# Performance work log

Measured on AMD Instinct MI355X. Metric: run time of the kernel, lower is better.

Reference implementation:

```python
import jax, jax.numpy as jnp
import numpy as np

B, N, C_IN, C_OUT, K = 8, 2048, 64, 128, 20
EPS = 1e-5  # BatchNorm2d default eps


def setup_inputs() -> dict:
    key = jax.random.key(0)
    k1, k2 = jax.random.split(key, 2)
    x = jax.random.normal(k1, (B, C_IN, N), dtype=jnp.float32)
    fan_in = 2 * C_IN
    W = jax.random.normal(k2, (C_OUT, 2 * C_IN), dtype=jnp.float32) / np.sqrt(fan_in).astype(np.float32)
    b = jnp.zeros((C_OUT,), jnp.float32)
    gamma = jnp.ones((C_OUT,), jnp.float32)
    beta = jnp.zeros((C_OUT,), jnp.float32)
    return {"x": x, "W": W, "b": b, "gamma": gamma, "beta": beta}


def reference(x, W, b, gamma, beta):
    # x: (B, C_in, N) -> points (B, N, C_in)
    pts = jnp.transpose(x, (0, 2, 1))
    # pairwise squared L2 distances (B, N, N)
    sq = jnp.sum(pts * pts, axis=-1)
    dist = sq[:, :, None] + sq[:, None, :] - 2.0 * jnp.einsum('bnc,bmc->bnm', pts, pts)
    # knn: top-k of negated distance -> k nearest neighbors (includes self)
    _, nn_idx = jax.lax.top_k(-dist, K)  # (B, N, K)
    # gather neighbor features per batch: (B, N, K, C_in)
    neigh = jax.vmap(lambda p, i: p[i])(pts, nn_idx)
    central = pts[:, :, None, :]  # (B, N, 1, C_in)
    edge = jnp.concatenate(
        [jnp.broadcast_to(central, neigh.shape), neigh - central], axis=-1
    )  # (B, N, K, 2*C_in)
    # 1x1 conv == channelwise linear: (B, N, K, C_out)
    y = jnp.einsum('bnkc,oc->bnko', edge, W) + b
    # BatchNorm2d (training mode): stats over batch + spatial dims, biased var
    mean = jnp.mean(y, axis=(0, 1, 2))
    var = jnp.var(y, axis=(0, 1, 2))
    y = (y - mean) * jax.lax.rsqrt(var + EPS) * gamma + beta
    y = jax.nn.relu(y)
    y = jnp.max(y, axis=2)  # max over k neighbors -> (B, N, C_out)
    return jnp.transpose(y, (0, 2, 1))[..., None]  # (B, C_out, N, 1)
```

## Files before the change

kernel.cpp:

```cpp
#include <hip/hip_runtime.h>
#include <cstdint>
#include <cstddef>

#define NPTS 2048
#define BATCH 8
#define CIN 64
#define CO 128
#define KNN 20
#define KSEL 24
#define NSPLIT 4
#define MKP 25

typedef short s16x8 __attribute__((ext_vector_type(8)));
typedef unsigned short u16x8 __attribute__((ext_vector_type(8)));
typedef float f32x4 __attribute__((ext_vector_type(4)));

__device__ inline unsigned short f2bf_rne(float x) {
  unsigned u = __float_as_uint(x);
  unsigned r = (u + 0x7FFFu + ((u >> 16) & 1u)) >> 16;
  return (unsigned short)r;
}
__device__ inline float bf2f(unsigned short h) {
  return __uint_as_float(((unsigned)h) << 16);
}
__device__ inline unsigned med3u(unsigned a, unsigned b, unsigned c) {
  unsigned d;
  asm("v_med3_u32 %0, %1, %2, %3" : "=v"(d) : "v"(a), "v"(b), "v"(c));
  return d;
}

__global__ __launch_bounds__(256) void prep_kernel(
    const float* __restrict__ x, float* __restrict__ P,
    unsigned short* __restrict__ PG, float* __restrict__ SQ,
    float* __restrict__ STATS) {
  __shared__ float tile[64 * 33];
  const int b = blockIdx.y, hb = blockIdx.x;
  const int n0 = hb * 32;
  const int tid = threadIdx.x;
  if (b == 0 && hb == 0) {
    for (int t = tid; t < 5 * CO; t += 256) STATS[t] = 0.f;
  }
  const float* xb = x + (size_t)b * CIN * NPTS;
#pragma unroll
  for (int j = 0; j < 8; ++j) {
    int e = j * 256 + tid;
    int c = e >> 5, nl = e & 31;
    tile[c * 33 + nl] = xb[(size_t)c * NPTS + n0 + nl];
  }
  __syncthreads();
  float* Pb = P + (size_t)b * NPTS * CIN;
#pragma unroll
  for (int j = 0; j < 8; ++j) {
    int e = j * 256 + tid;
    int nl = e >> 6, c = e & 63;
    Pb[(size_t)(n0 + nl) * CIN + c] = tile[c * 33 + nl];
  }
  if (tid < 32) {
    float acc = 0.f;
#pragma unroll
    for (int c = 0; c < 64; ++c) {
      float v = tile[c * 33 + tid];
      acc = fmaf(v, v, acc);
    }
    SQ[(size_t)b * NPTS + n0 + tid] = acc;
  }
  const size_t tbase = (size_t)(b * 32 + (n0 >> 6)) * 8192;
  {
    const int rl = tid >> 3, kc = tid & 7;
    const int grow = (n0 & 63) + rl;
    const int frag = ((grow >> 4) << 1) | (kc >> 2);
    const int lidx = (grow & 15) | ((kc & 3) << 4);
    s16x8 hi8, lo8;
#pragma unroll
    for (int e = 0; e < 8; ++e) {
      float v = tile[(kc * 8 + e) * 33 + rl];
      unsigned short hb_ = f2bf_rne(v);
      float hf = bf2f(hb_);
      unsigned short lb = f2bf_rne(v - hf);
      hi8[e] = (short)hb_;
      lo8[e] = (short)lb;
    }
    size_t co = (size_t)(frag * 64 + lidx) * 8;
    *(s16x8*)(PG + tbase + co) = hi8;
    *(s16x8*)(PG + tbase + 4096 + co) = lo8;
  }
}

__global__ __launch_bounds__(256, 4) void knn_part_kernel(
    const unsigned short* __restrict__ PG, const float* __restrict__ SQ,
    unsigned* __restrict__ POOLS) {
  const int b = blockIdx.z;
  const int cs = blockIdx.y;
  const int n0 = blockIdx.x * 64;
  const int tid = threadIdx.x;
  const int lane = tid & 63, w = tid >> 6;
  const int qi = w * 16 + (lane & 15);
  const int sub = lane >> 4;
  const int T0 = cs * 8;

  __shared__ unsigned mk[64 * 4 * MKP];

  const size_t tqb = (size_t)(b * 32 + (n0 >> 6)) * 8192;
  const s16x8 qhi0 = *(const s16x8*)(PG + tqb + (size_t)((w * 2 + 0) * 64 + lane) * 8);
  const s16x8 qhi1 = *(const s16x8*)(PG + tqb + (size_t)((w * 2 + 1) * 64 + lane) * 8);
  const s16x8 qlo0 = *(const s16x8*)(PG + tqb + 4096 + (size_t)((w * 2 + 0) * 64 + lane) * 8);
  const s16x8 qlo1 = *(const s16x8*)(PG + tqb + 4096 + (size_t)((w * 2 + 1) * 64 + lane) * 8);

  unsigned hk[KSEL];
#pragma unroll
  for (int s = 0; s < KSEL; ++s) hk[s] = 0xFFFFFFFFu;

#pragma unroll 1
  for (int t = 0; t < 8; ++t) {
    const int T = T0 + t;
    const unsigned short* tb = PG + (size_t)(b * 32 + T) * 8192;
#pragma unroll
    for (int rt = 0; rt < 4; ++rt) {
      const s16x8 ahi0 = *(const s16x8*)(tb + (size_t)((rt * 2 + 0) * 64 + lane) * 8);
      const s16x8 ahi1 = *(const s16x8*)(tb + (size_t)((rt * 2 + 1) * 64 + lane) * 8);
      const s16x8 alo0 = *(const s16x8*)(tb + 4096 + (size_t)((rt * 2 + 0) * 64 + lane) * 8);
      const s16x8 alo1 = *(const s16x8*)(tb + 4096 + (size_t)((rt * 2 + 1) * 64 + lane) * 8);
      f32x4 acc0 = {0.f, 0.f, 0.f, 0.f};
      f32x4 acc1 = {0.f, 0.f, 0.f, 0.f};
      acc0 = __builtin_amdgcn_mfma_f32_16x16x32_bf16(alo0, qhi0, acc0, 0, 0, 0);
      acc1 = __builtin_amdgcn_mfma_f32_16x16x32_bf16(alo1, qhi1, acc1, 0, 0, 0);
      acc0 = __builtin_amdgcn_mfma_f32_16x16x32_bf16(ahi0, qlo0, acc0, 0, 0, 0);
      acc1 = __builtin_amdgcn_mfma_f32_16x16x32_bf16(ahi1, qlo1, acc1, 0, 0, 0);
      acc0 = __builtin_amdgcn_mfma_f32_16x16x32_bf16(ahi0, qhi0, acc0, 0, 0, 0);
      acc1 = __builtin_amdgcn_mfma_f32_16x16x32_bf16(ahi1, qhi1, acc1, 0, 0, 0);
      const float4 sq4 = *(const float4*)(SQ + b * NPTS + T * 64 + rt * 16 + sub * 4);
      const float sqa[4] = {sq4.x, sq4.y, sq4.z, sq4.w};
      const int mbase = T * 64 + rt * 16 + sub * 4;
#pragma unroll
      for (int r = 0; r < 4; ++r) {
        float d = fmaf(acc0[r] + acc1[r], -2.0f, sqa[r]);
        unsigned u = __float_as_uint(d);
        unsigned ord = u ^ (unsigned)(((int)u >> 31) | 0x80000000);
        unsigned key = (ord & 0xFFFFF800u) | (unsigned)(mbase + r);
#pragma unroll
        for (int s = KSEL - 1; s >= 1; --s) hk[s] = med3u(hk[s - 1], hk[s], key);
        hk[0] = hk[0] < key ? hk[0] : key;
      }
    }
  }

#pragma unroll
  for (int s = 0; s < KSEL; ++s) mk[(qi * 4 + sub) * MKP + s] = hk[s];
  __syncthreads();

  if (sub == 0) {
    const unsigned* bl = mk + qi * 4 * MKP;
    unsigned* pq = POOLS + ((size_t)(b * NPTS + n0 + qi) * NSPLIT + cs) * KSEL;
    int p0 = 0, p1 = 0, p2 = 0, p3 = 0;
#pragma unroll 1
    for (int s = 0; s < KSEL; ++s) {
      unsigned k0 = (p0 < KSEL) ? bl[0 * MKP + p0] : 0xFFFFFFFFu;
      unsigned k1 = (p1 < KSEL) ? bl[1 * MKP + p1] : 0xFFFFFFFFu;
      unsigned k2 = (p2 < KSEL) ? bl[2 * MKP + p2] : 0xFFFFFFFFu;
      unsigned k3 = (p3 < KSEL) ? bl[3 * MKP + p3] : 0xFFFFFFFFu;
      unsigned bk = k0; int bs = 0;
      if (k1 < bk) { bk = k1; bs = 1; }
      if (k2 < bk) { bk = k2; bs = 2; }
      if (k3 < bk) { bk = k3; bs = 3; }
      pq[s] = bk;
      if (bs == 0) ++p0; else if (bs == 1) ++p1; else if (bs == 2) ++p2; else ++p3;
    }
  }
}

__global__ __launch_bounds__(256) void merge_proj_kernel(
    const float* __restrict__ P, const float* __restrict__ W,
    const unsigned* __restrict__ POOLS, int* __restrict__ IDX,
    float* __restrict__ U, unsigned short* __restrict__ Vh) {
  __shared__ __align__(16) char smem[35072];
  const int tid = threadIdx.x;

  if (blockIdx.x < 1024) {
    const int blk = blockIdx.x;
    const int r0 = (blk >> 2) * 64;
    const int o0 = (blk & 3) * 32;
    const int og = tid & 3;
    const int nl = tid >> 2;
    float* Pt = (float*)smem;
    float* Wu_s = Pt + 64 * 65;
    float* Wd_s = Wu_s + 64 * 36;

#pragma unroll
    for (int j = 0; j < 16; ++j) {
      int e = j * 256 + tid;
      int c = e & 63, rl = e >> 6;
      Pt[rl * 65 + c] = P[((size_t)(r0 + rl) << 6) + c];
    }
#pragma unroll
    for (int j = 0; j < 8; ++j) {
      int e = j * 256 + tid;
      int c = e & 63, ol = e >> 6;
      float w1 = W[(size_t)(o0 + ol) * 128 + c];
      float w2 = W[(size_t)(o0 + ol) * 128 + 64 + c];
      Wu_s[c * 36 + ol] = w1 - w2;
      Wd_s[c * 36 + ol] = w2;
    }
    __syncthreads();

    float au[8] = {0,0,0,0,0,0,0,0};
    float av[8] = {0,0,0,0,0,0,0,0};
#pragma unroll 4
    for (int c = 0; c < 64; ++c) {
      float p = Pt[nl * 65 + c];
      const float* wu = Wu_s + c * 36 + og * 8;
      const float* wd = Wd_s + c * 36 + og * 8;
      float4 u0 = *(const float4*)wu;
      float4 u1 = *(const float4*)(wu + 4);
      float4 dd0 = *(const float4*)wd;
      float4 dd1 = *(const float4*)(wd + 4);
      au[0] = fmaf(p, u0.x, au[0]); au[1] = fmaf(p, u0.y, au[1]);
      au[2] = fmaf(p, u0.z, au[2]); au[3] = fmaf(p, u0.w, au[3]);
      au[4] = fmaf(p, u1.x, au[4]); au[5] = fmaf(p, u1.y, au[5]);
      au[6] = fmaf(p, u1.z, au[6]); au[7] = fmaf(p, u1.w, au[7]);
      av[0] = fmaf(p, dd0.x, av[0]); av[1] = fmaf(p, dd0.y, av[1]);
      av[2] = fmaf(p, dd0.z, av[2]); av[3] = fmaf(p, dd0.w, av[3]);
      av[4] = fmaf(p, dd1.x, av[4]); av[5] = fmaf(p, dd1.y, av[5]);
      av[6] = fmaf(p, dd1.z, av[6]); av[7] = fmaf(p, dd1.w, av[7]);
    }
    size_t ob = (size_t)(r0 + nl) * CO + o0 + og * 8;
    float4 s0 = {au[0], au[1], au[2], au[3]};
    float4 s1 = {au[4], au[5], au[6], au[7]};
    *(float4*)(U + ob) = s0;
    *(float4*)(U + ob + 4) = s1;
    u16x8 hv;
#pragma unroll
    for (int j = 0; j < 8; ++j) hv[j] = f2bf_rne(av[j]);
    *(u16x8*)(Vh + ob) = hv;
  } else {
    const int mblk = blockIdx.x - 1024;
    const int qi = tid >> 3, st = tid & 7;
    const int r0 = mblk * 32;
    const int r = r0 + qi;
    const int b = r >> 11;

    unsigned* lists = (unsigned*)smem;
    unsigned* pool = lists + 32 * NSPLIT * KSEL;
    double* cd = (double*)(pool + 32 * KSEL);

    {
      const unsigned* src = POOLS + (size_t)r0 * NSPLIT * KSEL;
      for (int t = tid; t < 32 * NSPLIT * KSEL; t += 256) lists[t] = src[t];
    }
    __syncthreads();

    if (st == 0) {
      const unsigned* bl = lists + qi * NSPLIT * KSEL;
      unsigned* pq = pool + qi * KSEL;
      int p0 = 0, p1 = 0, p2 = 0, p3 = 0;
#pragma unroll 1
      for (int s = 0; s < KSEL; ++s) {
        unsigned k0 = (p0 < KSEL) ? bl[0 * KSEL + p0] : 0xFFFFFFFFu;
        unsigned k1 = (p1 < KSEL) ? bl[1 * KSEL + p1] : 0xFFFFFFFFu;
        unsigned k2 = (p2 < KSEL) ? bl[2 * KSEL + p2] : 0xFFFFFFFFu;
        unsigned k3 = (p3 < KSEL) ? bl[3 * KSEL + p3] : 0xFFFFFFFFu;
        unsigned bk = k0; int bs = 0;
        if (k1 < bk) { bk = k1; bs = 1; }
        if (k2 < bk) { bk = k2; bs = 2; }
        if (k3 < bk) { bk = k3; bs = 3; }
        pq[s] = bk;
        if (bs == 0) ++p0; else if (bs == 1) ++p1; else if (bs == 2) ++p2; else ++p3;
      }
    }
    __syncthreads();

    const float* qrow = P + ((size_t)r << 6);
    float4 q4[16];
#pragma unroll
    for (int t = 0; t < 16; ++t) q4[t] = ((const float4*)qrow)[t];
#pragma unroll 1
    for (int j = 0; j < 3; ++j) {
      int cand = st * 3 + j;
      unsigned key = pool[qi * KSEL + cand];
      int m = (int)(key & 0x7FFu);
      const float* prow = P + ((size_t)(b * NPTS + m) << 6);
      double a0 = 0.0, a1 = 0.0;
#pragma unroll
      for (int t = 0; t < 16; ++t) {
        float4 pv = ((const float4*)prow)[t];
        double d0 = (double)pv.x - (double)q4[t].x;
        double d1 = (double)pv.y - (double)q4[t].y;
        double d2 = (double)pv.z - (double)q4[t].z;
        double d3 = (double)pv.w - (double)q4[t].w;
        a0 = fma(d1, d1, fma(d0, d0, a0));
        a1 = fma(d3, d3, fma(d2, d2, a1));
      }
      cd[qi * KSEL + cand] = a0 + a1;
    }
    __syncthreads();

    int* op = IDX + (size_t)r * KNN;
#pragma unroll 1
    for (int j = 0; j < 3; ++j) {
      int cand = st * 3 + j;
      double dv = cd[qi * KSEL + cand];
      int iv = (int)(pool[qi * KSEL + cand] & 0x7FFu);
      int rk = 0;
#pragma unroll 1
      for (int t = 0; t < KSEL; ++t) {
        double dt = cd[qi * KSEL + t];
        int it = (int)(pool[qi * KSEL + t] & 0x7FFu);
        rk += ((dt < dv) || (dt == dv && it < iv)) ? 1 : 0;
      }
      if (rk < KNN) op[rk] = iv;
    }
  }
}

__global__ __launch_bounds__(256) void gstats_kernel(
    const float* __restrict__ U, const unsigned short* __restrict__ Vh,
    const int* __restrict__ IDX, unsigned short* __restrict__ Zh,
    float* __restrict__ STATS) {
  const int r0 = blockIdx.x * 16;
  const int tid = threadIdx.x;
  const int og = tid & 15, nl = tid >> 4;
  const int r = r0 + nl;
  const int b = r >> 11;
  const unsigned short* Vb = Vh + ((size_t)b << 11) * CO;

  __shared__ int ii[16 * KNN];
  __shared__ float red[4][5][128];

  for (int t = tid; t < 16 * KNN; t += 256) ii[t] = IDX[(size_t)r0 * KNN + t];
  __syncthreads();

  float vmax[8], svr[8], svvr[8];
#pragma unroll
  for (int j = 0; j < 8; ++j) { vmax[j] = -3.4e38f; svr[j] = 0.f; svvr[j] = 0.f; }
#pragma unroll 4
  for (int k = 0; k < KNN; ++k) {
    int idx = ii[nl * KNN + k];
    u16x8 hv = *(const u16x8*)(Vb + (size_t)idx * CO + og * 8);
#pragma unroll
    for (int j = 0; j < 8; ++j) {
      float v = bf2f((unsigned short)hv[j]);
      vmax[j] = fmaxf(vmax[j], v);
      svr[j] += v;
      svvr[j] = fmaf(v, v, svvr[j]);
    }
  }
  size_t ob = (size_t)r * CO + og * 8;
  float4 u0 = *(const float4*)(U + ob);
  float4 u1 = *(const float4*)(U + ob + 4);
  float uu[8] = {u0.x, u0.y, u0.z, u0.w, u1.x, u1.y, u1.z, u1.w};
  u16x8 zh;
#pragma unroll
  for (int j = 0; j < 8; ++j) zh[j] = f2bf_rne(uu[j] + vmax[j]);
  *(u16x8*)(Zh + ob) = zh;

  float pu[8], puu[8], psv[8], pusv[8], psvv[8];
#pragma unroll
  for (int j = 0; j < 8; ++j) {
    pu[j] = uu[j];
    puu[j] = uu[j] * uu[j];
    psv[j] = svr[j];
    pusv[j] = uu[j] * svr[j];
    psvv[j] = svvr[j];
  }
#pragma unroll
  for (int j = 0; j < 8; ++j) {
    pu[j]   += __shfl_xor(pu[j], 16);   pu[j]   += __shfl_xor(pu[j], 32);
    puu[j]  += __shfl_xor(puu[j], 16);  puu[j]  += __shfl_xor(puu[j], 32);
    psv[j]  += __shfl_xor(psv[j], 16);  psv[j]  += __shfl_xor(psv[j], 32);
    pusv[j] += __shfl_xor(pusv[j], 16); pusv[j] += __shfl_xor(pusv[j], 32);
    psvv[j] += __shfl_xor(psvv[j], 16); psvv[j] += __shfl_xor(psvv[j], 32);
  }
  const int w = tid >> 6;
  if ((tid & 0x30) == 0) {
#pragma unroll
    for (int j = 0; j < 8; ++j) {
      int c = og * 8 + j;
      red[w][0][c] = pu[j];  red[w][1][c] = puu[j];  red[w][2][c] = psv[j];
      red[w][3][c] = pusv[j]; red[w][4][c] = psvv[j];
    }
  }
  __syncthreads();
  if (tid < 128) {
#pragma unroll
    for (int s = 0; s < 5; ++s) {
      float v4 = red[0][s][tid] + red[1][s][tid] + red[2][s][tid] + red[3][s][tid];
      atomicAdd(&STATS[s * CO + tid], v4);
    }
  }
}

__global__ __launch_bounds__(256) void out_kernel(
    const unsigned short* __restrict__ Zh, const float* __restrict__ STATS,
    const float* __restrict__ bias, const float* __restrict__ gamma,
    const float* __restrict__ beta, float* __restrict__ out) {
  const int n0 = blockIdx.x * 64, o0 = blockIdx.y * 32, b = blockIdx.z;
  const int tid = threadIdx.x;
  __shared__ float tile[64 * 33];
  __shared__ float fs[32], ft[32];
  if (tid < 32) {
    const int o = o0 + tid;
    const float M = (float)(BATCH * NPTS * KNN);
    const float Kf = (float)KNN;
    float su = STATS[0 * CO + o], suu = STATS[1 * CO + o], ssv = STATS[2 * CO + o];
    float susv = STATS[3 * CO + o], ssvv = STATS[4 * CO + o];
    float bo = bias[o];
    float lin = (Kf * su + ssv) / M;
    float mean = lin + bo;
    float ey2 = (Kf * suu + ssvv + 2.0f * susv) / M + 2.0f * bo * lin + bo * bo;
    float var = ey2 - mean * mean;
    float scale = gamma[o] * rsqrtf(var + 1e-5f);
    fs[tid] = scale;
    ft[tid] = (bo - mean) * scale + beta[o];
  }
#pragma unroll
  for (int j = 0; j < 8; ++j) {
    int e = j * 256 + tid;
    int ol = e & 31, nl = e >> 5;
    tile[nl * 33 + ol] = bf2f(Zh[(size_t)(b * NPTS + n0 + nl) * CO + o0 + ol]);
  }
  __syncthreads();
#pragma unroll
  for (int j = 0; j < 8; ++j) {
    int e = j * 256 + tid;
    int nl = e & 63, ol = e >> 6;
    float v = fmaf(tile[nl * 33 + ol], fs[ol], ft[ol]);
    out[(size_t)(b * CO + o0 + ol) * NPTS + n0 + nl] = fmaxf(v, 0.0f);
  }
}

extern "C" void kernel_launch(void* const* d_in, const int* in_sizes, int n_in,
                              void* d_out, int out_size, void* d_ws, size_t ws_size,
                              hipStream_t stream) {
  const float* x = (const float*)d_in[0];
  const float* W = (const float*)d_in[1];
  const float* bias = (const float*)d_in[2];
  const float* gamma = (const float*)d_in[3];
  const float* beta = (const float*)d_in[4];
  float* out = (float*)d_out;
  float* ws = (float*)d_ws;

  const size_t NR = (size_t)BATCH * NPTS;
  size_t off = 0;
  float* P = ws + off;                      off += NR * CIN;
  unsigned short* PG = (unsigned short*)(ws + off); off += NR * CIN;
  float* SQ = ws + off;                     off += NR;
  int* IDX = (int*)(ws + off);              off += NR * KNN;
  float* U = ws + off;                      off += NR * CO;
  unsigned short* Vh = (unsigned short*)(ws + off); off += NR * CO / 2;
  unsigned* POOLS = (unsigned*)(ws + off);  off += NR * NSPLIT * KSEL;
  float* STATS = ws + off;                  off += 5 * CO;
  unsigned short* Zh = (unsigned short*)ws;
  if (ws_size < off * sizeof(float)) return;

  prep_kernel<<<dim3(NPTS / 32, BATCH), 256, 0, stream>>>(x, P, PG, SQ, STATS);
  knn_part_kernel<<<dim3(NPTS / 64, NSPLIT, BATCH), 256, 0, stream>>>(PG, SQ, POOLS);
  merge_proj_kernel<<<dim3(1024 + NR / 32), 256, 0, stream>>>(P, W, POOLS, IDX, U, Vh);
  gstats_kernel<<<dim3(NR / 16), 256, 0, stream>>>(U, Vh, IDX, Zh, STATS);
  out_kernel<<<dim3(NPTS / 64, CO / 32, BATCH), 256, 0, stream>>>(Zh, STATS, bias, gamma, beta, out);
}
```

Measured before the change: 135.7 us.

## Store U projection in bf16 and chain kNN MFMAs into one accumulator

The U projection buffer is now written and read as bf16 instead of fp32, which halves its global memory traffic between merge_proj and gstats. In the kNN kernel the two independent MFMA accumulators become a single serial chain, which removes one add per element and some registers. The kNN kernel also drops its minimum-occupancy launch bound. Rounding U to bf16 loses precision in the BN statistics and outputs, and the serial MFMA chain creates a longer dependency between instructions.

```diff
diff --git a/kernel.cpp b/kernel.cpp
--- a/kernel.cpp
+++ b/kernel.cpp
@@ -86,7 +86,7 @@
   }
 }
 
-__global__ __launch_bounds__(256, 4) void knn_part_kernel(
+__global__ __launch_bounds__(256) void knn_part_kernel(
     const unsigned short* __restrict__ PG, const float* __restrict__ SQ,
     unsigned* __restrict__ POOLS) {
   const int b = blockIdx.z;
@@ -120,20 +120,19 @@
       const s16x8 ahi1 = *(const s16x8*)(tb + (size_t)((rt * 2 + 1) * 64 + lane) * 8);
       const s16x8 alo0 = *(const s16x8*)(tb + 4096 + (size_t)((rt * 2 + 0) * 64 + lane) * 8);
       const s16x8 alo1 = *(const s16x8*)(tb + 4096 + (size_t)((rt * 2 + 1) * 64 + lane) * 8);
-      f32x4 acc0 = {0.f, 0.f, 0.f, 0.f};
-      f32x4 acc1 = {0.f, 0.f, 0.f, 0.f};
-      acc0 = __builtin_amdgcn_mfma_f32_16x16x32_bf16(alo0, qhi0, acc0, 0, 0, 0);
-      acc1 = __builtin_amdgcn_mfma_f32_16x16x32_bf16(alo1, qhi1, acc1, 0, 0, 0);
-      acc0 = __builtin_amdgcn_mfma_f32_16x16x32_bf16(ahi0, qlo0, acc0, 0, 0, 0);
-      acc1 = __builtin_amdgcn_mfma_f32_16x16x32_bf16(ahi1, qlo1, acc1, 0, 0, 0);
-      acc0 = __builtin_amdgcn_mfma_f32_16x16x32_bf16(ahi0, qhi0, acc0, 0, 0, 0);
-      acc1 = __builtin_amdgcn_mfma_f32_16x16x32_bf16(ahi1, qhi1, acc1, 0, 0, 0);
+      f32x4 acc = {0.f, 0.f, 0.f, 0.f};
+      acc = __builtin_amdgcn_mfma_f32_16x16x32_bf16(alo0, qhi0, acc, 0, 0, 0);
+      acc = __builtin_amdgcn_mfma_f32_16x16x32_bf16(ahi0, qlo0, acc, 0, 0, 0);
+      acc = __builtin_amdgcn_mfma_f32_16x16x32_bf16(ahi0, qhi0, acc, 0, 0, 0);
+      acc = __builtin_amdgcn_mfma_f32_16x16x32_bf16(alo1, qhi1, acc, 0, 0, 0);
+      acc = __builtin_amdgcn_mfma_f32_16x16x32_bf16(ahi1, qlo1, acc, 0, 0, 0);
+      acc = __builtin_amdgcn_mfma_f32_16x16x32_bf16(ahi1, qhi1, acc, 0, 0, 0);
       const float4 sq4 = *(const float4*)(SQ + b * NPTS + T * 64 + rt * 16 + sub * 4);
       const float sqa[4] = {sq4.x, sq4.y, sq4.z, sq4.w};
       const int mbase = T * 64 + rt * 16 + sub * 4;
 #pragma unroll
       for (int r = 0; r < 4; ++r) {
-        float d = fmaf(acc0[r] + acc1[r], -2.0f, sqa[r]);
+        float d = fmaf(acc[r], -2.0f, sqa[r]);
         unsigned u = __float_as_uint(d);
         unsigned ord = u ^ (unsigned)(((int)u >> 31) | 0x80000000);
         unsigned key = (ord & 0xFFFFF800u) | (unsigned)(mbase + r);
@@ -171,7 +170,7 @@
 __global__ __launch_bounds__(256) void merge_proj_kernel(
     const float* __restrict__ P, const float* __restrict__ W,
     const unsigned* __restrict__ POOLS, int* __restrict__ IDX,
-    float* __restrict__ U, unsigned short* __restrict__ Vh) {
+    unsigned short* __restrict__ Uh, unsigned short* __restrict__ Vh) {
   __shared__ __align__(16) char smem[35072];
   const int tid = threadIdx.x;
 
@@ -223,13 +222,10 @@
       av[6] = fmaf(p, dd1.z, av[6]); av[7] = fmaf(p, dd1.w, av[7]);
     }
     size_t ob = (size_t)(r0 + nl) * CO + o0 + og * 8;
-    float4 s0 = {au[0], au[1], au[2], au[3]};
-    float4 s1 = {au[4], au[5], au[6], au[7]};
-    *(float4*)(U + ob) = s0;
-    *(float4*)(U + ob + 4) = s1;
-    u16x8 hv;
-#pragma unroll
-    for (int j = 0; j < 8; ++j) hv[j] = f2bf_rne(av[j]);
+    u16x8 hu, hv;
+#pragma unroll
+    for (int j = 0; j < 8; ++j) { hu[j] = f2bf_rne(au[j]); hv[j] = f2bf_rne(av[j]); }
+    *(u16x8*)(Uh + ob) = hu;
     *(u16x8*)(Vh + ob) = hv;
   } else {
     const int mblk = blockIdx.x - 1024;
@@ -312,7 +308,7 @@
 }
 
 __global__ __launch_bounds__(256) void gstats_kernel(
-    const float* __restrict__ U, const unsigned short* __restrict__ Vh,
+    const unsigned short* __restrict__ Uh, const unsigned short* __restrict__ Vh,
     const int* __restrict__ IDX, unsigned short* __restrict__ Zh,
     float* __restrict__ STATS) {
   const int r0 = blockIdx.x * 16;
@@ -344,9 +340,10 @@
     }
   }
   size_t ob = (size_t)r * CO + og * 8;
-  float4 u0 = *(const float4*)(U + ob);
-  float4 u1 = *(const float4*)(U + ob + 4);
-  float uu[8] = {u0.x, u0.y, u0.z, u0.w, u1.x, u1.y, u1.z, u1.w};
+  u16x8 hu = *(const u16x8*)(Uh + ob);
+  float uu[8];
+#pragma unroll
+  for (int j = 0; j < 8; ++j) uu[j] = bf2f((unsigned short)hu[j]);
   u16x8 zh;
 #pragma unroll
   for (int j = 0; j < 8; ++j) zh[j] = f2bf_rne(uu[j] + vmax[j]);
@@ -444,7 +441,7 @@
   unsigned short* PG = (unsigned short*)(ws + off); off += NR * CIN;
   float* SQ = ws + off;                     off += NR;
   int* IDX = (int*)(ws + off);              off += NR * KNN;
-  float* U = ws + off;                      off += NR * CO;
+  unsigned short* Uh = (unsigned short*)(ws + off); off += NR * CO / 2;
   unsigned short* Vh = (unsigned short*)(ws + off); off += NR * CO / 2;
   unsigned* POOLS = (unsigned*)(ws + off);  off += NR * NSPLIT * KSEL;
   float* STATS = ws + off;                  off += 5 * CO;
@@ -453,7 +450,7 @@
 
   prep_kernel<<<dim3(NPTS / 32, BATCH), 256, 0, stream>>>(x, P, PG, SQ, STATS);
   knn_part_kernel<<<dim3(NPTS / 64, NSPLIT, BATCH), 256, 0, stream>>>(PG, SQ, POOLS);
-  merge_proj_kernel<<<dim3(1024 + NR / 32), 256, 0, stream>>>(P, W, POOLS, IDX, U, Vh);
-  gstats_kernel<<<dim3(NR / 16), 256, 0, stream>>>(U, Vh, IDX, Zh, STATS);
+  merge_proj_kernel<<<dim3(1024 + NR / 32), 256, 0, stream>>>(P, W, POOLS, IDX, Uh, Vh);
+  gstats_kernel<<<dim3(NR / 16), 256, 0, stream>>>(Uh, Vh, IDX, Zh, STATS);
   out_kernel<<<dim3(NPTS / 64, CO / 32, BATCH), 256, 0, stream>>>(Zh, STATS, bias, gamma, beta, out);
 }
```

New measurement: 136.3 us. No clear change (+0.4%).
